# Optimization experiments

Hardware: AMD Instinct MI355X
Metric: run time of the kernel (lower is better)

The kernel has to match this reference:

```python
import jax, jax.numpy as jnp
import numpy as np

N, T, GX, GY, GQ = 16, 64, 256, 256, 256   # solutions, timesteps, source grid, query grid
H, D = 4, 8                                 # attention heads / head dim
SIGMA = 0.2
LY_MIN, LY_MAX = 30.0, 120.0
CU_REF, NI_REF = 0.0029, 0.0018
LX = 100.0


def setup_inputs() -> dict:
    key = jax.random.key(0)
    ks = jax.random.split(key, 7)
    lys = jax.random.uniform(ks[0], (N,), minval=40.0, maxval=110.0)
    ccu = jax.random.uniform(ks[1], (N,), minval=0.001, maxval=CU_REF)
    cni = jax.random.uniform(ks[2], (N,), minval=0.0005, maxval=NI_REF)
    params = jnp.stack([lys, ccu, cni], axis=1).astype(jnp.float32)  # [N,3] raw (Ly, C_Cu, C_Ni)
    x_grids = jnp.tile(jnp.linspace(0.0, LX, GX, dtype=jnp.float32)[None], (N, 1))      # [N,GX]
    y_grids = lys[:, None] * jnp.linspace(0.0, 1.0, GY, dtype=jnp.float32)[None]        # [N,GY]
    c1_src = jax.random.normal(ks[3], (N, T, GX, GY), dtype=jnp.float32)
    c2_src = jax.random.normal(ks[4], (N, T, GX, GY), dtype=jnp.float32)
    Wq_w = 0.1 * jax.random.normal(ks[5], (H * D, 3), dtype=jnp.float32)
    Wk_w = 0.1 * jax.random.normal(ks[6], (H * D, 3), dtype=jnp.float32)
    Wq_b = jnp.zeros((H * D,), jnp.float32)
    Wk_b = jnp.zeros((H * D,), jnp.float32)
    return dict(c1_src=c1_src, c2_src=c2_src, x_grids=x_grids, y_grids=y_grids,
                params=params, Wq_w=Wq_w, Wq_b=Wq_b, Wk_w=Wk_w, Wk_b=Wk_b,
                ly_target=jnp.float32(75.0), c_cu_target=jnp.float32(0.0029),
                c_ni_target=jnp.float32(0.0018))


def _bilinear(c, xg, yg, qx, qy):
    """Linear interp on rectilinear grid, fill_value=0 out of bounds.
    c: [T,Gx,Gy], xg: [Gx], yg: [Gy], qx/qy: [P] -> [T,P]."""
    ix = jnp.clip(jnp.searchsorted(xg, qx, side='right') - 1, 0, xg.shape[0] - 2)
    iy = jnp.clip(jnp.searchsorted(yg, qy, side='right') - 1, 0, yg.shape[0] - 2)
    x0, x1 = xg[ix], xg[ix + 1]
    y0, y1 = yg[iy], yg[iy + 1]
    fx = (qx - x0) / (x1 - x0)
    fy = (qy - y0) / (y1 - y0)
    c00 = c[:, ix, iy]
    c10 = c[:, ix + 1, iy]
    c01 = c[:, ix, iy + 1]
    c11 = c[:, ix + 1, iy + 1]
    v = ((1 - fx) * (1 - fy)) * c00 + (fx * (1 - fy)) * c10 \
        + ((1 - fx) * fy) * c01 + (fx * fy) * c11
    inb = (qx >= xg[0]) & (qx <= xg[-1]) & (qy >= yg[0]) & (qy <= yg[-1])
    return jnp.where(inb[None, :], v, 0.0)


def _forward(c1_src, c2_src, x_grids, y_grids, params, Wq_w, Wq_b, Wk_w, Wk_b,
             ly_target, c_cu_target, c_ni_target):
    # --- parameter normalization (same constants as original) ---
    p = jnp.stack([(params[:, 0] - LY_MIN) / (LY_MAX - LY_MIN),
                   params[:, 1] / CU_REF,
                   params[:, 2] / NI_REF], axis=1)                     # [N,3]
    tgt = jnp.stack([(ly_target - LY_MIN) / (LY_MAX - LY_MIN),
                     c_cu_target / CU_REF,
                     c_ni_target / NI_REF])[None, :]                   # [1,3]
    # --- tiny multi-head attention weights ---
    q = (tgt @ Wq_w.T + Wq_b).reshape(1, H, D)
    k = (p @ Wk_w.T + Wk_b).reshape(p.shape[0], H, D)
    attn = jnp.einsum('nhd,mhd->nmh', k, q) / np.sqrt(D).astype(np.float32)  # [N,1,H]
    attn_w = jax.nn.softmax(attn, axis=0).mean(axis=2).squeeze(1)            # [N]
    # --- gaussian spatial weights ---
    sw = jnp.exp(-0.5 * jnp.sum(((p - tgt) / SIGMA) ** 2, axis=1))
    sw = sw / sw.sum()
    w = attn_w * sw
    w = w / w.sum()
    w = jax.lax.stop_gradient(w)  # original detaches weights before interpolation
    # --- batched bilinear interpolation onto target grid ---
    Lx = x_grids[0, -1]
    unit = jnp.linspace(0.0, 1.0, GQ, dtype=jnp.float32)
    X, Y = jnp.meshgrid(unit * Lx, unit * ly_target, indexing='ij')    # [GQ,GQ]
    qx, qy = X.ravel(), Y.ravel()                                      # [P]
    ys = y_grids * (ly_target / params[:, 0])[:, None]                 # per-solution rescaled Y grids
    interp = jax.vmap(_bilinear, in_axes=(0, 0, 0, None, None))        # -> [N,T,P]
    c1 = jnp.einsum('n,ntp->tp', w, interp(c1_src, x_grids, ys, qx, qy)).reshape(T, GQ, GQ)
    c2 = jnp.einsum('n,ntp->tp', w, interp(c2_src, x_grids, ys, qx, qy)).reshape(T, GQ, GQ)
    # --- boundary conditions ---
    c1 = c1.at[:, :, 0].set(c_cu_target)
    c2 = c2.at[:, :, -1].set(c_ni_target)
    return jnp.stack([c1, c2]), w


def reference(c1_src, c2_src, x_grids, y_grids, params, Wq_w, Wq_b, Wk_w, Wk_b,
              ly_target, c_cu_target, c_ni_target):
    return _forward(c1_src, c2_src, x_grids, y_grids, params, Wq_w, Wq_b, Wk_w, Wk_b,
                    ly_target, c_cu_target, c_ni_target)
```

## Files before the change

### kernel.cpp

```cpp
#include <hip/hip_runtime.h>

#define N_SRC 16
#define T_DIM 64
#define GXD 256
#define GYD 256
#define GQD 256
#define HN 4
#define DN 8
#define TI 8
#define OUT_C_ELEMS (2 * T_DIM * GQD * GQD)

#define WS_IY   0
#define WS_WY0  16384
#define WS_WY1  32768
#define WS_IX   49152
#define WS_WX0  50176
#define WS_WX1  51200

__device__ __forceinline__ float unitv(int i) {
    return (i == GQD - 1) ? 1.0f : (float)i * (1.0f / 255.0f);
}

__global__ __launch_bounds__(256) void table_kernel(
    const float* __restrict__ xg, const float* __restrict__ yg,
    const float* __restrict__ params,
    const float* __restrict__ Wq_w, const float* __restrict__ Wq_b,
    const float* __restrict__ Wk_w, const float* __restrict__ Wk_b,
    const float* __restrict__ lyt_p, const float* __restrict__ ccut_p,
    const float* __restrict__ cnit_p,
    float* __restrict__ out_w, char* __restrict__ ws)
{
    __shared__ float xg_sm[GXD];
    __shared__ float ys_sm[N_SRC][GYD];
    __shared__ float w_sm[N_SRC];

    const int tid = threadIdx.x;
    const float lyt = *lyt_p;

    xg_sm[tid] = xg[tid];
    #pragma unroll
    for (int n = 0; n < N_SRC; ++n) {
        float s = lyt / params[n * 3 + 0];
        ys_sm[n][tid] = yg[n * GYD + tid] * s;
    }

    if (tid == 0) {
        const float ccut = *ccut_p, cnit = *cnit_p;
        float tgt[3];
        tgt[0] = (lyt - 30.0f) / 90.0f;
        tgt[1] = ccut / 0.0029f;
        tgt[2] = cnit / 0.0018f;
        float q[HN * DN];
        for (int hd = 0; hd < HN * DN; ++hd)
            q[hd] = tgt[0] * Wq_w[hd * 3 + 0] + tgt[1] * Wq_w[hd * 3 + 1] + tgt[2] * Wq_w[hd * 3 + 2] + Wq_b[hd];
        float p[N_SRC][3];
        float attn[N_SRC][HN];
        for (int n = 0; n < N_SRC; ++n) {
            p[n][0] = (params[n * 3 + 0] - 30.0f) / 90.0f;
            p[n][1] = params[n * 3 + 1] / 0.0029f;
            p[n][2] = params[n * 3 + 2] / 0.0018f;
            for (int h = 0; h < HN; ++h) {
                float acc = 0.0f;
                for (int d = 0; d < DN; ++d) {
                    int hd = h * DN + d;
                    float kv = p[n][0] * Wk_w[hd * 3 + 0] + p[n][1] * Wk_w[hd * 3 + 1] + p[n][2] * Wk_w[hd * 3 + 2] + Wk_b[hd];
                    acc += kv * q[hd];
                }
                attn[n][h] = acc / sqrtf(8.0f);
            }
        }
        float aw[N_SRC];
        for (int n = 0; n < N_SRC; ++n) aw[n] = 0.0f;
        for (int h = 0; h < HN; ++h) {
            float m = attn[0][h];
            for (int n = 1; n < N_SRC; ++n) m = fmaxf(m, attn[n][h]);
            float e[N_SRC], s = 0.0f;
            for (int n = 0; n < N_SRC; ++n) { e[n] = expf(attn[n][h] - m); s += e[n]; }
            for (int n = 0; n < N_SRC; ++n) aw[n] += e[n] / s;
        }
        for (int n = 0; n < N_SRC; ++n) aw[n] *= (1.0f / (float)HN);
        float sw[N_SRC], ss = 0.0f;
        for (int n = 0; n < N_SRC; ++n) {
            float d0 = (p[n][0] - tgt[0]) / 0.2f;
            float d1 = (p[n][1] - tgt[1]) / 0.2f;
            float d2 = (p[n][2] - tgt[2]) / 0.2f;
            sw[n] = expf(-0.5f * (d0 * d0 + d1 * d1 + d2 * d2));
            ss += sw[n];
        }
        float w[N_SRC], wsum = 0.0f;
        for (int n = 0; n < N_SRC; ++n) { w[n] = aw[n] * (sw[n] / ss); wsum += w[n]; }
        for (int n = 0; n < N_SRC; ++n) {
            float wf = w[n] / wsum;
            w_sm[n] = wf;
            out_w[n] = wf;
        }
    }
    __syncthreads();

    int*   iy_tab  = (int*)  (ws + WS_IY);
    float* wy0_tab = (float*)(ws + WS_WY0);
    float* wy1_tab = (float*)(ws + WS_WY1);
    int*   ix_tab  = (int*)  (ws + WS_IX);
    float* wx0_tab = (float*)(ws + WS_WX0);
    float* wx1_tab = (float*)(ws + WS_WX1);

    const int j = tid;
    const float qy = unitv(j) * lyt;
    #pragma unroll
    for (int n = 0; n < N_SRC; ++n) {
        int lo = 0, hi = GYD;
        while (lo < hi) { int mid = (lo + hi) >> 1; if (ys_sm[n][mid] <= qy) lo = mid + 1; else hi = mid; }
        int idx = lo - 1;
        idx = idx < 0 ? 0 : (idx > GYD - 2 ? GYD - 2 : idx);
        float y0 = ys_sm[n][idx], y1 = ys_sm[n][idx + 1];
        float fy = (qy - y0) / (y1 - y0);
        float vy = (qy >= ys_sm[n][0] && qy <= ys_sm[n][GYD - 1]) ? 1.0f : 0.0f;
        float wn = w_sm[n] * vy;
        iy_tab [n * GQD + j] = idx;
        wy0_tab[n * GQD + j] = wn * (1.0f - fy);
        wy1_tab[n * GQD + j] = wn * fy;
    }

    const float Lx = xg_sm[GXD - 1];
    const float qx = unitv(tid) * Lx;
    int lo = 0, hi = GXD;
    while (lo < hi) { int mid = (lo + hi) >> 1; if (xg_sm[mid] <= qx) lo = mid + 1; else hi = mid; }
    int ixi = lo - 1;
    ixi = ixi < 0 ? 0 : (ixi > GXD - 2 ? GXD - 2 : ixi);
    const float x0 = xg_sm[ixi], x1 = xg_sm[ixi + 1];
    const float fx = (qx - x0) / (x1 - x0);
    const float vx = (qx >= xg_sm[0] && qx <= xg_sm[GXD - 1]) ? 1.0f : 0.0f;
    ix_tab [tid] = ixi;
    wx0_tab[tid] = vx * (1.0f - fx);
    wx1_tab[tid] = vx * fx;
}

__global__ __launch_bounds__(256, 4) void fused_kernel(
    const float* __restrict__ c1, const float* __restrict__ c2,
    const float* __restrict__ ccut_p, const float* __restrict__ cnit_p,
    const char* __restrict__ ws, float* __restrict__ out)
{
    __shared__ int   ixb_sm[TI];
    __shared__ float wx0_sm[TI], wx1_sm[TI];

    const int tid = threadIdx.x;
    const int j = tid;
    const int i0 = blockIdx.x * TI;
    const int t = blockIdx.y;

    const int*   iy_tab  = (const int*)  (ws + WS_IY);
    const float* wy0_tab = (const float*)(ws + WS_WY0);
    const float* wy1_tab = (const float*)(ws + WS_WY1);

    if (tid < TI) {
        ixb_sm[tid] = ((const int*)  (ws + WS_IX)) [i0 + tid];
        wx0_sm[tid] = ((const float*)(ws + WS_WX0))[i0 + tid];
        wx1_sm[tid] = ((const float*)(ws + WS_WX1))[i0 + tid];
    }
    __syncthreads();

    int   rq  [TI];
    float wx0r[TI], wx1r[TI];
    #pragma unroll
    for (int ii = 0; ii < TI; ++ii) {
        rq  [ii] = ixb_sm[ii] * GYD;
        wx0r[ii] = wx0_sm[ii];
        wx1r[ii] = wx1_sm[ii];
    }

    float acc1[TI], acc2[TI];
    #pragma unroll
    for (int ii = 0; ii < TI; ++ii) { acc1[ii] = 0.0f; acc2[ii] = 0.0f; }

    const size_t tbase = (size_t)t * (GXD * GYD);
    const float* b1 = c1 + tbase;
    const float* b2 = c2 + tbase;

    #pragma unroll 4
    for (int n = 0; n < N_SRC; ++n) {
        const int   iy  = iy_tab [n * GQD + j];
        const float wy0 = wy0_tab[n * GQD + j];
        const float wy1 = wy1_tab[n * GQD + j];
        const float* p1 = b1 + (size_t)n * ((size_t)T_DIM * GXD * GYD);
        const float* p2 = b2 + (size_t)n * ((size_t)T_DIM * GXD * GYD);
        #pragma unroll
        for (int ii = 0; ii < TI; ++ii) {
            const int o = rq[ii] + iy;
            const float a00 = p1[o];
            const float a01 = p1[o + 1];
            const float a10 = p1[o + GYD];
            const float a11 = p1[o + GYD + 1];
            const float b00 = p2[o];
            const float b01 = p2[o + 1];
            const float b10 = p2[o + GYD];
            const float b11 = p2[o + GYD + 1];
            const float v0 = wy0 * a00 + wy1 * a01;
            const float v1 = wy0 * a10 + wy1 * a11;
            acc1[ii] += wx0r[ii] * v0 + wx1r[ii] * v1;
            const float u0 = wy0 * b00 + wy1 * b01;
            const float u1 = wy0 * b10 + wy1 * b11;
            acc2[ii] += wx0r[ii] * u0 + wx1r[ii] * u1;
        }
    }

    const float ccut = *ccut_p, cnit = *cnit_p;
    #pragma unroll
    for (int ii = 0; ii < TI; ++ii) {
        const int i = i0 + ii;
        float o1 = acc1[ii];
        float o2 = acc2[ii];
        if (j == 0)       o1 = ccut;
        if (j == GQD - 1) o2 = cnit;
        __builtin_nontemporal_store(o1, &out[((size_t)t * GQD + i) * GQD + j]);
        __builtin_nontemporal_store(o2, &out[(((size_t)T_DIM + t) * GQD + i) * GQD + j]);
    }
}

extern "C" void kernel_launch(void* const* d_in, const int* in_sizes, int n_in,
                              void* d_out, int out_size, void* d_ws, size_t ws_size,
                              hipStream_t stream) {
    const float* c1     = (const float*)d_in[0];
    const float* c2     = (const float*)d_in[1];
    const float* xg     = (const float*)d_in[2];
    const float* yg     = (const float*)d_in[3];
    const float* params = (const float*)d_in[4];
    const float* Wq_w   = (const float*)d_in[5];
    const float* Wq_b   = (const float*)d_in[6];
    const float* Wk_w   = (const float*)d_in[7];
    const float* Wk_b   = (const float*)d_in[8];
    const float* lyt    = (const float*)d_in[9];
    const float* ccut   = (const float*)d_in[10];
    const float* cnit   = (const float*)d_in[11];
    float* out = (float*)d_out;
    float* out_w = out + OUT_C_ELEMS;
    char* ws = (char*)d_ws;

    table_kernel<<<1, 256, 0, stream>>>(xg, yg, params, Wq_w, Wq_b, Wk_w, Wk_b,
                                        lyt, ccut, cnit, out_w, ws);
    dim3 grid(GQD / TI, T_DIM);
    fused_kernel<<<grid, 256, 0, stream>>>(c1, c2, ccut, cnit, ws, out);
}
```

Baseline: 646.2 us.

## Stage source row bands into LDS with async global_load_lds multi-buffer pipeline

Replaces the per-thread scattered global gathers with a cooperative copy of a 10-row band of each source plane into shared memory. The copy uses direct global-to-LDS loads, with four buffers and three planes in flight. Each thread then interpolates along y once per row and reuses those row values across the 8 output rows, choosing neighbours by the x-index offset. This targets redundant global traffic and load latency. The cost is 48KB of LDS per block, a hand-managed vmcnt and barrier schedule, and the assumption that the 8 query rows fall within a 10-row band.

Result: faster. 595.7 us (-7.8%).

```diff
diff --git a/kernel.cpp b/kernel.cpp
--- a/kernel.cpp
+++ b/kernel.cpp
@@ -8,6 +8,13 @@
 #define HN 4
 #define DN 8
 #define TI 8
+#define ROWS 12
+#define ROWSV 10
+#define NB 4
+#define NPLANES (2 * N_SRC)
+#define CHPP 3
+#define USED_CHUNKS (ROWSV * 64)
+#define PLANE_STRIDE ((size_t)T_DIM * GXD * GYD)
 #define OUT_C_ELEMS (2 * T_DIM * GQD * GQD)
 
 #define WS_IY   0
@@ -135,13 +142,18 @@
     wx1_tab[tid] = vx * fx;
 }
 
+__device__ __forceinline__ void gl_lds16(const float* g, float* l) {
+    __builtin_amdgcn_global_load_lds(
+        (const __attribute__((address_space(1))) void*)g,
+        (__attribute__((address_space(3))) void*)l, 16, 0, 0);
+}
+
 __global__ __launch_bounds__(256, 4) void fused_kernel(
     const float* __restrict__ c1, const float* __restrict__ c2,
     const float* __restrict__ ccut_p, const float* __restrict__ cnit_p,
     const char* __restrict__ ws, float* __restrict__ out)
 {
-    __shared__ int   ixb_sm[TI];
-    __shared__ float wx0_sm[TI], wx1_sm[TI];
+    __shared__ float buf[NB][ROWS * GYD];
 
     const int tid = threadIdx.x;
     const int j = tid;
@@ -151,57 +163,105 @@
     const int*   iy_tab  = (const int*)  (ws + WS_IY);
     const float* wy0_tab = (const float*)(ws + WS_WY0);
     const float* wy1_tab = (const float*)(ws + WS_WY1);
-
-    if (tid < TI) {
-        ixb_sm[tid] = ((const int*)  (ws + WS_IX)) [i0 + tid];
-        wx0_sm[tid] = ((const float*)(ws + WS_WX0))[i0 + tid];
-        wx1_sm[tid] = ((const float*)(ws + WS_WX1))[i0 + tid];
-    }
-    __syncthreads();
-
-    int   rq  [TI];
+    const int*   ix_tab  = (const int*)  (ws + WS_IX);
+    const float* wx0_tab = (const float*)(ws + WS_WX0);
+    const float* wx1_tab = (const float*)(ws + WS_WX1);
+
+    const int x0r = ix_tab[i0];
+    int   dsel[TI];
     float wx0r[TI], wx1r[TI];
     #pragma unroll
     for (int ii = 0; ii < TI; ++ii) {
-        rq  [ii] = ixb_sm[ii] * GYD;
-        wx0r[ii] = wx0_sm[ii];
-        wx1r[ii] = wx1_sm[ii];
-    }
+        int d = ix_tab[i0 + ii] - x0r - ii;
+        dsel[ii] = d < -1 ? -1 : (d > 1 ? 1 : d);
+        wx0r[ii] = wx0_tab[i0 + ii];
+        wx1r[ii] = wx1_tab[i0 + ii];
+    }
+
+    int   iyr [N_SRC];
+    float wy0r[N_SRC], wy1r[N_SRC];
+    #pragma unroll
+    for (int n = 0; n < N_SRC; ++n) {
+        iyr [n] = iy_tab [n * GQD + j];
+        wy0r[n] = wy0_tab[n * GQD + j];
+        wy1r[n] = wy1_tab[n * GQD + j];
+    }
+
+    size_t soff[CHPP];
+    int    ldst[CHPP];
+    #pragma unroll
+    for (int k = 0; k < CHPP; ++k) {
+        int c  = tid + k * 256;
+        int cc = c < USED_CHUNKS ? c : USED_CHUNKS - 1;
+        int grow = x0r + (cc >> 6);
+        grow = grow > GXD - 1 ? GXD - 1 : grow;
+        soff[k] = (size_t)grow * GYD + ((cc & 63) << 2);
+        ldst[k] = c << 2;
+    }
+
+    const size_t pbase = (size_t)t * (GXD * GYD);
 
     float acc1[TI], acc2[TI];
     #pragma unroll
     for (int ii = 0; ii < TI; ++ii) { acc1[ii] = 0.0f; acc2[ii] = 0.0f; }
 
-    const size_t tbase = (size_t)t * (GXD * GYD);
-    const float* b1 = c1 + tbase;
-    const float* b2 = c2 + tbase;
-
-    #pragma unroll 4
-    for (int n = 0; n < N_SRC; ++n) {
-        const int   iy  = iy_tab [n * GQD + j];
-        const float wy0 = wy0_tab[n * GQD + j];
-        const float wy1 = wy1_tab[n * GQD + j];
-        const float* p1 = b1 + (size_t)n * ((size_t)T_DIM * GXD * GYD);
-        const float* p2 = b2 + (size_t)n * ((size_t)T_DIM * GXD * GYD);
-        #pragma unroll
-        for (int ii = 0; ii < TI; ++ii) {
-            const int o = rq[ii] + iy;
-            const float a00 = p1[o];
-            const float a01 = p1[o + 1];
-            const float a10 = p1[o + GYD];
-            const float a11 = p1[o + GYD + 1];
-            const float b00 = p2[o];
-            const float b01 = p2[o + 1];
-            const float b10 = p2[o + GYD];
-            const float b11 = p2[o + GYD + 1];
-            const float v0 = wy0 * a00 + wy1 * a01;
-            const float v1 = wy0 * a10 + wy1 * a11;
-            acc1[ii] += wx0r[ii] * v0 + wx1r[ii] * v1;
-            const float u0 = wy0 * b00 + wy1 * b01;
-            const float u1 = wy0 * b10 + wy1 * b11;
-            acc2[ii] += wx0r[ii] * u0 + wx1r[ii] * u1;
-        }
-    }
+#define STAGE(q) do {                                                          \
+    const float* _s = (((q) & 1) ? c2 : c1) + pbase                            \
+                      + (size_t)((q) >> 1) * PLANE_STRIDE;                     \
+    float* _l = &buf[(q) & (NB - 1)][0];                                       \
+    gl_lds16(_s + soff[0], _l + ldst[0]);                                      \
+    gl_lds16(_s + soff[1], _l + ldst[1]);                                      \
+    gl_lds16(_s + soff[2], _l + ldst[2]);                                      \
+} while (0)
+
+#define CONSUME(q, ACC) do {                                                   \
+    const float* _B = &buf[(q) & (NB - 1)][0];                                 \
+    const int _iy = iyr[(q) >> 1];                                             \
+    const float _w0 = wy0r[(q) >> 1], _w1 = wy1r[(q) >> 1];                    \
+    float _rv[ROWSV];                                                          \
+    _Pragma("unroll")                                                          \
+    for (int _r = 0; _r < ROWSV; ++_r)                                         \
+        _rv[_r] = _w0 * _B[_r * GYD + _iy] + _w1 * _B[_r * GYD + _iy + 1];     \
+    _Pragma("unroll")                                                          \
+    for (int _ii = 0; _ii < TI; ++_ii) {                                       \
+        const int _im1 = _ii > 0 ? _ii - 1 : 0;                                \
+        const int _ip2 = _ii + 2 < ROWSV ? _ii + 2 : ROWSV - 1;                \
+        const int _d = dsel[_ii];                                              \
+        float _lo = _d == 0 ? _rv[_ii]     : (_d < 0 ? _rv[_im1] : _rv[_ii+1]);\
+        float _hi = _d == 0 ? _rv[_ii + 1] : (_d < 0 ? _rv[_ii]  : _rv[_ip2]); \
+        ACC[_ii] += wx0r[_ii] * _lo + wx1r[_ii] * _hi;                         \
+    }                                                                          \
+} while (0)
+
+#define WAITQ(q) do {                                                          \
+    if ((q) < NPLANES - 2)       asm volatile("s_waitcnt vmcnt(6)" ::: "memory"); \
+    else if ((q) == NPLANES - 2) asm volatile("s_waitcnt vmcnt(3)" ::: "memory"); \
+    else                         asm volatile("s_waitcnt vmcnt(0)" ::: "memory"); \
+} while (0)
+
+#define PLANE(q) do {                                                          \
+    WAITQ(q);                                                                  \
+    __builtin_amdgcn_s_barrier();                                              \
+    __builtin_amdgcn_sched_barrier(0);                                         \
+    if ((q) + 3 < NPLANES) STAGE((q) + 3);                                     \
+    if (((q) & 1) == 0) CONSUME((q), acc1); else CONSUME((q), acc2);           \
+} while (0)
+
+    STAGE(0); STAGE(1); STAGE(2);
+
+    PLANE(0);  PLANE(1);  PLANE(2);  PLANE(3);
+    PLANE(4);  PLANE(5);  PLANE(6);  PLANE(7);
+    PLANE(8);  PLANE(9);  PLANE(10); PLANE(11);
+    PLANE(12); PLANE(13); PLANE(14); PLANE(15);
+    PLANE(16); PLANE(17); PLANE(18); PLANE(19);
+    PLANE(20); PLANE(21); PLANE(22); PLANE(23);
+    PLANE(24); PLANE(25); PLANE(26); PLANE(27);
+    PLANE(28); PLANE(29); PLANE(30); PLANE(31);
+
+#undef PLANE
+#undef WAITQ
+#undef CONSUME
+#undef STAGE
 
     const float ccut = *ccut_p, cnit = *cnit_p;
     #pragma unroll
```
